# Kernel tuning notes

Hardware: AMD Instinct MI355X
Metric: run time of the kernel (lower is better)

Reference implementation:

```python
import jax, jax.numpy as jnp
import numpy as np

ROPE_BASE = 10000.0

def _rope_tables(T, head_dim, dtype):
    inv_freq = 1.0 / (ROPE_BASE ** (jnp.arange(0, head_dim, 2, dtype=jnp.float32) / head_dim))
    freqs = jnp.arange(T, dtype=jnp.float32)[:, None] * inv_freq[None, :]  # (T, hd/2)
    freqs = jnp.repeat(freqs, 2, axis=-1)  # (T, hd) interleaved (lucidrains-style)
    return jnp.cos(freqs).astype(dtype), jnp.sin(freqs).astype(dtype)

def _rotate_half(x):
    # interleaved pairs: (..., d) -> (-x2, x1) interleaved
    x = x.reshape(x.shape[:-1] + (-1, 2))
    x1, x2 = x[..., 0], x[..., 1]
    return jnp.stack((-x2, x1), axis=-1).reshape(x.shape[:-2] + (-1,))

def _apply_rope(x, cos, sin):
    # x: (B, H, T, hd); cos/sin: (T, hd)
    return x * cos[None, None] + _rotate_half(x) * sin[None, None]

def setup_inputs() -> dict:
    key = jax.random.key(0)
    k1, k2, k3 = jax.random.split(key, 3)
    B, T, C = 4, 2048, 1024
    x = jax.random.normal(k1, (B, T, C), dtype=jnp.float32)
    W_attn = jax.random.normal(k2, (C, 3 * C), dtype=jnp.float32) * 0.02
    W_proj = jax.random.normal(k3, (C, C), dtype=jnp.float32) * 0.02
    return {"x": x, "W_attn": W_attn, "W_proj": W_proj}

def reference(x, W_attn, W_proj):
    B, T, C = x.shape
    n_head = 16
    hd = C // n_head
    qkv = x @ W_attn  # (B, T, 3C)
    q, k, v = jnp.split(qkv, 3, axis=-1)
    # (B, T, H, hd) -> (B, H, T, hd)
    q = q.reshape(B, T, n_head, hd).transpose(0, 2, 1, 3)
    k = k.reshape(B, T, n_head, hd).transpose(0, 2, 1, 3)
    v = v.reshape(B, T, n_head, hd).transpose(0, 2, 1, 3)
    cos, sin = _rope_tables(T, hd, x.dtype)
    q = _apply_rope(q, cos, sin)
    k = _apply_rope(k, cos, sin)
    att = jnp.einsum('bhqd,bhkd->bhqk', q, k) * (1.0 / jnp.sqrt(jnp.array(hd, dtype=x.dtype)))
    causal = jnp.tril(jnp.ones((T, T), dtype=bool))
    att = jnp.where(causal[None, None], att, jnp.array(-jnp.inf, dtype=att.dtype))
    att = jax.nn.softmax(att, axis=-1)
    y = jnp.einsum('bhqk,bhkd->bhqd', att, v)
    y = y.transpose(0, 2, 1, 3).reshape(B, T, C)
    return y @ W_proj
```

## Files before the change

kernel.cpp:

```cpp
#include <hip/hip_runtime.h>
#include <hip/hip_bf16.h>
#include <math.h>

#define BB 4
#define TT 2048
#define CC 1024
#define NH 16
#define HD 64
#define C3 3072
#define LDK 72

#define QSCALE 0.18033688011112042f

typedef __attribute__((ext_vector_type(8))) short bf16x8;
typedef __attribute__((ext_vector_type(4))) float f32x4;

__device__ __forceinline__ void gload_lds16(const __hip_bfloat16* g, __hip_bfloat16* s) {
    __builtin_amdgcn_global_load_lds((const __attribute__((address_space(1))) void*)g,
                                     (__attribute__((address_space(3))) void*)s, 16, 0, 0);
}

__global__ __launch_bounds__(256) void rope_tables(float2* __restrict__ tab) {
    int idx = blockIdx.x * 256 + threadIdx.x;
    int t = idx >> 5;
    int p = idx & 31;
    float invf = exp2f((float)p * (-13.287712379549449f / 32.0f));
    float ang = (float)t * invf;
    float s, c;
    sincosf(ang, &s, &c);
    tab[idx] = make_float2(c, s);
}

__global__ __launch_bounds__(256) void cast_bf16x8(const float* __restrict__ X,
                                                   __hip_bfloat16* __restrict__ Y) {
    size_t i = ((size_t)blockIdx.x * 256 + threadIdx.x) * 8;
    float4 a = *(const float4*)(X + i);
    float4 b = *(const float4*)(X + i + 4);
    __align__(16) __hip_bfloat16 tmp[8];
    tmp[0] = __float2bfloat16(a.x);
    tmp[1] = __float2bfloat16(a.y);
    tmp[2] = __float2bfloat16(a.z);
    tmp[3] = __float2bfloat16(a.w);
    tmp[4] = __float2bfloat16(b.x);
    tmp[5] = __float2bfloat16(b.y);
    tmp[6] = __float2bfloat16(b.z);
    tmp[7] = __float2bfloat16(b.w);
    *(bf16x8*)(Y + i) = *(bf16x8*)tmp;
}

__global__ __launch_bounds__(256) void wtrans(const float* __restrict__ W,
                                              __hip_bfloat16* __restrict__ Wt,
                                              int K, int N) {
    __shared__ float st[64][65];
    const int n0 = blockIdx.x * 64;
    const int k0 = blockIdx.y * 64;
    const int tid = threadIdx.x;
    const int r = tid >> 4;
    const int c4 = (tid & 15) * 4;
#pragma unroll
    for (int p = 0; p < 4; ++p) {
        int k = p * 16 + r;
        float4 v = *(const float4*)(W + (size_t)(k0 + k) * N + n0 + c4);
        st[c4 + 0][k] = v.x;
        st[c4 + 1][k] = v.y;
        st[c4 + 2][k] = v.z;
        st[c4 + 3][k] = v.w;
    }
    __syncthreads();
    const int rr = tid >> 3;
    const int cc = (tid & 7) * 8;
#pragma unroll
    for (int p = 0; p < 2; ++p) {
        int n = p * 32 + rr;
        __align__(16) __hip_bfloat16 tmp[8];
#pragma unroll
        for (int j = 0; j < 8; ++j) tmp[j] = __float2bfloat16(st[n][cc + j]);
        *(bf16x8*)(Wt + (size_t)(n0 + n) * K + k0 + cc) = *(bf16x8*)tmp;
    }
}

#define CA0 0
#define CA1 1
#define CB0 2
#define CB1 3

#define BAR() __builtin_amdgcn_s_barrier()
#define SB0() __builtin_amdgcn_sched_barrier(0)
#define WAIT_LGKM0() do { asm volatile("s_waitcnt lgkmcnt(0)" ::: "memory"); SB0(); } while (0)
#define WAIT_VM4()   do { asm volatile("s_waitcnt vmcnt(4)" ::: "memory");  SB0(); } while (0)
#define WAIT_VM0()   do { asm volatile("s_waitcnt vmcnt(0)" ::: "memory");  SB0(); } while (0)

#define CLAMP_TS(x) ((x) < NTILE ? (x) : (x) - 2)

#define STAGE(gbase, h, ts, buf, cid) do {                                            \
    const __hip_bfloat16* _s = (gbase) + (size_t)((h) * 128 + w * 16) * K + (ts) * 64; \
    __hip_bfloat16* _d = &lds[buf][cid][w * 1024];                                    \
    gload_lds16(_s, _d);                                                              \
    gload_lds16(_s + 32, _d + 512);                                                   \
} while (0)

#define FRAGP(buf, cid, rowsub, ks)                                                   \
    ((const bf16x8*)((const char*)&lds[buf][cid][0] +                                 \
        (((rowsub) * 2 + (ks)) << 10) + (l16 << 6) + swzoff))

#define READ_A(buf, mi) do {                                                          \
    _Pragma("unroll") for (int _m = 0; _m < 4; ++_m)                                  \
    _Pragma("unroll") for (int _k = 0; _k < 2; ++_k)                                  \
        af[_m][_k] = *FRAGP(buf, wm, (mi) * 4 + _m, _k);                              \
} while (0)

#define READ_B(buf, ni) do {                                                          \
    _Pragma("unroll") for (int _n = 0; _n < 2; ++_n)                                  \
    _Pragma("unroll") for (int _k = 0; _k < 2; ++_k)                                  \
        bfr[(ni) * 2 + _n][_k] =                                                      \
            *FRAGP(buf, 2 + (wn >> 1), (wn & 1) * 4 + (ni) * 2 + _n, _k);             \
} while (0)

#define MFMA_Q(mb, nb) do {                                                           \
    __builtin_amdgcn_s_setprio(1);                                                    \
    _Pragma("unroll") for (int _m = 0; _m < 4; ++_m)                                  \
    _Pragma("unroll") for (int _n = 0; _n < 2; ++_n)                                  \
    _Pragma("unroll") for (int _k = 0; _k < 2; ++_k)                                  \
        acc[(mb) * 4 + _m][(nb) * 2 + _n] = __builtin_amdgcn_mfma_f32_16x16x32_bf16(  \
            af[_m][_k], bfr[(nb) * 2 + _n][_k], acc[(mb) * 4 + _m][(nb) * 2 + _n],    \
            0, 0, 0);                                                                 \
    __builtin_amdgcn_s_setprio(0);                                                    \
} while (0)

#define HALF_ITER(BUF, T12, B12, T34, B34) do {                                       \
                                                                 \
    READ_A(BUF, 0);                                                                   \
    READ_B(BUF, 0);                                                                   \
    STAGE(Bb, 1, CLAMP_TS(T12), B12, CB1);                                            \
    BAR(); WAIT_LGKM0();                                                              \
    MFMA_Q(0, 0);                                                                     \
    BAR();                                                                            \
                                                                 \
    READ_B(BUF, 1);                                                                   \
    STAGE(Ab, 1, CLAMP_TS(T12), B12, CA1);                                            \
    BAR(); WAIT_LGKM0();                                                              \
    MFMA_Q(0, 1);                                                                     \
    BAR();                                                                            \
                                                                 \
    READ_A(BUF, 1);                                                                   \
    STAGE(Bb, 0, CLAMP_TS(T34), B34, CB0);                                            \
    BAR(); WAIT_LGKM0();                                                              \
    MFMA_Q(1, 0);                                                                     \
    BAR();                                                                            \
                                                                 \
    STAGE(Ab, 0, CLAMP_TS(T34), B34, CA0);                                            \
    BAR(); WAIT_LGKM0();                                                              \
    MFMA_Q(1, 1);                                                                     \
    WAIT_VM4();                                                                       \
    BAR(); SB0();                                                                     \
} while (0)

#define GEMM256_BODY                                                                  \
    __shared__ __align__(16) __hip_bfloat16 lds[2][4][8192];             \
    const int tid = threadIdx.x;                                                      \
    const int w = tid >> 6;                                                           \
    const int lane = tid & 63;                                                        \
    const int l16 = lane & 15;                                                        \
    const int quad = lane >> 4;                                                       \
    const int wm = w >> 2;                                                            \
    const int wn = w & 3;                                                             \
    const int swzoff = ((quad * 8) ^ ((l16 & 8) << 1)) << 1;                          \
    const int bm0 = blockIdx.y * 256;                                                 \
    const int bn0 = blockIdx.x * 256;                                                 \
    const int NTILE = K >> 6;                                                         \
    const size_t laneOff = (size_t)(lane >> 2) * K +                                  \
                           (((lane & 3) * 8) ^ ((lane >> 5) << 4));                   \
    const __hip_bfloat16* Ab = A + (size_t)bm0 * K + laneOff;                         \
    const __hip_bfloat16* Bb = Bt + (size_t)bn0 * K + laneOff;                        \
    f32x4 acc[8][4] = {};                                                             \
             \
    STAGE(Bb, 0, 0, 0, CB0);                                                          \
    STAGE(Ab, 0, 0, 0, CA0);                                                          \
    STAGE(Bb, 1, 0, 0, CB1);                                                          \
    STAGE(Ab, 1, 0, 0, CA1);                                                          \
    STAGE(Bb, 0, 1, 1, CB0);                                                          \
    STAGE(Ab, 0, 1, 1, CA0);                                                          \
    WAIT_VM4();                                                                       \
    BAR(); SB0();                                                                     \
    for (int it = 0; it < NTILE / 2; ++it) {                                          \
        const int t = it * 2;                                                         \
        bf16x8 af[4][2], bfr[4][2];                                                   \
        HALF_ITER(0, t + 1, 1, t + 2, 0);                                             \
        HALF_ITER(1, t + 2, 0, t + 3, 1);                                             \
    }

__global__ __launch_bounds__(512) void gemm256_qkv_rope(const __hip_bfloat16* __restrict__ A,
                                                        const __hip_bfloat16* __restrict__ Bt,
                                                        const float2* __restrict__ tab,
                                                        __hip_bfloat16* __restrict__ C,
                                                        int M, int N, int K) {
    GEMM256_BODY

    if (bn0 < 2048) {
        const float qsc = (bn0 < 1024) ? QSCALE : 1.0f;
        const float sgn = (l16 & 1) ? 1.0f : -1.0f;
#pragma unroll
        for (int mt = 0; mt < 8; ++mt) {
            int row = bm0 + wm * 128 + mt * 16 + quad * 4;
#pragma unroll
            for (int nt = 0; nt < 4; ++nt) {
                int col = bn0 + wn * 64 + nt * 16 + l16;
                int p2 = nt * 8 + (l16 >> 1);
#pragma unroll
                for (int r = 0; r < 4; ++r) {
                    float own = acc[mt][nt][r];
                    float part = __shfl_xor(own, 1);
                    int trow = (row + r) & (TT - 1);
                    float2 cs = tab[(trow << 5) + p2];
                    float res = (own * cs.x + sgn * part * cs.y) * qsc;
                    C[(size_t)(row + r) * N + col] = __float2bfloat16(res);
                }
            }
        }
    } else {
#pragma unroll
        for (int mt = 0; mt < 8; ++mt) {
            int row = bm0 + wm * 128 + mt * 16 + quad * 4;
#pragma unroll
            for (int nt = 0; nt < 4; ++nt) {
                int col = bn0 + wn * 64 + nt * 16 + l16;
#pragma unroll
                for (int r = 0; r < 4; ++r)
                    C[(size_t)(row + r) * N + col] = __float2bfloat16(acc[mt][nt][r]);
            }
        }
    }
}

__global__ __launch_bounds__(512) void gemm256_f32(const __hip_bfloat16* __restrict__ A,
                                                   const __hip_bfloat16* __restrict__ Bt,
                                                   float* __restrict__ C,
                                                   int M, int N, int K) {
    GEMM256_BODY
#pragma unroll
    for (int mt = 0; mt < 8; ++mt) {
        int row = bm0 + wm * 128 + mt * 16 + quad * 4;
#pragma unroll
        for (int nt = 0; nt < 4; ++nt) {
            int col = bn0 + wn * 64 + nt * 16 + l16;
#pragma unroll
            for (int r = 0; r < 4; ++r)
                C[(size_t)(row + r) * N + col] = acc[mt][nt][r];
        }
    }
}

__global__ __launch_bounds__(256) void vtranspose(const __hip_bfloat16* __restrict__ qkvb,
                                                  __hip_bfloat16* __restrict__ vtb) {
    __shared__ __align__(16) __hip_bfloat16 st[64][LDK];
    const int bh = blockIdx.x >> 5;
    const int tt = blockIdx.x & 31;
    const int b = bh >> 4;
    const int h = bh & 15;
    const int tid = threadIdx.x;
    const int row = tid >> 3;
    const int col8 = (tid & 7) * 8;

#pragma unroll
    for (int pass = 0; pass < 2; ++pass) {
        int t = pass * 32 + row;
        *(bf16x8*)(&st[t][col8]) =
            *(const bf16x8*)(qkvb + ((size_t)(b * TT + tt * 64 + t)) * C3 + 2 * CC + h * HD + col8);
    }
    __syncthreads();
#pragma unroll
    for (int pass = 0; pass < 2; ++pass) {
        int d = pass * 32 + row;
        __align__(16) __hip_bfloat16 tmp[8];
#pragma unroll
        for (int j = 0; j < 8; ++j) tmp[j] = st[col8 + j][d];
        *(bf16x8*)(vtb + ((size_t)bh * HD + d) * TT + tt * 64 + col8) = *(bf16x8*)tmp;
    }
}

__global__ __launch_bounds__(256) void attn_mfma6(const __hip_bfloat16* __restrict__ qkvb,
                                                  const __hip_bfloat16* __restrict__ vtb,
                                                  __hip_bfloat16* __restrict__ y) {
    __shared__ __align__(16) __hip_bfloat16 Kb[3][64 * 64];
    __shared__ __align__(16) __hip_bfloat16 Vb[3][64 * 64];
    __shared__ __align__(16) __hip_bfloat16 Ps[4][2][16 * 72];

    const int tid = threadIdx.x;
    const int w = tid >> 6;
    const int lane = tid & 63;
    const int l16 = lane & 15;
    const int quad = lane >> 4;
    const int swz = l16 & 7;

    const int bh = blockIdx.x >> 3;
    const int pr = blockIdx.x & 7;
    const int b = bh >> 4;
    const int h = bh & 15;

    const int sr = (lane >> 3) & 7;
    const int sc = lane & 7;
    const int klog = (sc ^ sr) * 8;

    const __hip_bfloat16* kbase = qkvb + (size_t)b * TT * C3 + CC + h * HD + klog;
    const __hip_bfloat16* vbase = vtb + (size_t)bh * HD * TT + klog;

#define ATTN_STAGE(t, bidx) do {                                                  \
    _Pragma("unroll")                                                             \
    for (int half = 0; half < 2; ++half) {                                        \
        int kr = w * 16 + half * 8 + sr;                                          \
        gload_lds16(kbase + (size_t)((t) * 64 + kr) * C3,                         \
                    Kb[bidx] + (w * 16 + half * 8) * 64);                         \
        gload_lds16(vbase + (size_t)kr * TT + (t) * 64,                           \
                    Vb[bidx] + (w * 16 + half * 8) * 64);                         \
    }                                                                             \
} while (0)

#pragma unroll
    for (int seg = 0; seg < 2; ++seg) {
        const int qblk = (seg == 0) ? (15 - pr) : pr;
        const int qb = qblk * 128;
        const int jtmax = 2 * qblk + 1;
        const int qn0 = qb + w * 32;
        const int qn1 = qn0 + 16;

        bf16x8 qf[2][2];
#pragma unroll
        for (int qt = 0; qt < 2; ++qt) {
            const __hip_bfloat16* qp = qkvb + (size_t)(b * TT + qn0 + qt * 16 + l16) * C3 + h * HD;
            qf[qt][0] = *(const bf16x8*)(qp + quad * 8);
            qf[qt][1] = *(const bf16x8*)(qp + 32 + quad * 8);
        }

        f32x4 O[2][4] = {};
        float l_q[2] = {0.f, 0.f};

        __syncthreads();
        ATTN_STAGE(0, 0);
        ATTN_STAGE(1, 1);

        int bcur = 0;
        for (int jt = 0; jt <= jtmax; ++jt) {
            if (jt < jtmax) { WAIT_VM4(); } else { WAIT_VM0(); }
            BAR(); SB0();

            if (jt + 2 <= jtmax) {
                const int bs = (bcur >= 1) ? (bcur - 1) : 2;
                ATTN_STAGE(jt + 2, bs);
            }

            const __hip_bfloat16* Kp = Kb[bcur];
            const __hip_bfloat16* Vp = Vb[bcur];

            const bool sk0 = (jt * 64 > qn0 + 15);
            const bool sk1 = (jt * 64 > qn1 + 15);

            if (!sk1) {
                f32x4 St[2][4] = {};
                __builtin_amdgcn_s_setprio(1);
#pragma unroll
                for (int ks = 0; ks < 2; ++ks) {
#pragma unroll
                    for (int mt = 0; mt < 4; ++mt) {
                        bf16x8 kf = *(const bf16x8*)(Kp + (mt * 16 + l16) * 64 +
                                                     ((ks * 4 + quad) ^ swz) * 8);
                        St[0][mt] = __builtin_amdgcn_mfma_f32_16x16x32_bf16(kf, qf[0][ks], St[0][mt], 0, 0, 0);
                        St[1][mt] = __builtin_amdgcn_mfma_f32_16x16x32_bf16(kf, qf[1][ks], St[1][mt], 0, 0, 0);
                    }
                }
                __builtin_amdgcn_s_setprio(0);

#pragma unroll
                for (int qt = 0; qt < 2; ++qt) {
                    const bool skq = qt == 0 ? sk0 : sk1;
                    if (skq) continue;
                    const int qn = qt == 0 ? qn0 : qn1;
                    if (jt * 64 + 63 > qn) {
#pragma unroll
                        for (int mt = 0; mt < 4; ++mt) {
#pragma unroll
                            for (int r = 0; r < 4; ++r) {
                                int key = jt * 64 + mt * 16 + quad * 4 + r;
                                if (key > qn + l16) St[qt][mt][r] = -__builtin_inff();
                            }
                        }
                    }
                    float sum = 0.f;
#pragma unroll
                    for (int mt = 0; mt < 4; ++mt) {
                        float e0 = exp2f(St[qt][mt][0]);
                        float e1 = exp2f(St[qt][mt][1]);
                        float e2 = exp2f(St[qt][mt][2]);
                        float e3 = exp2f(St[qt][mt][3]);
                        sum += (e0 + e1) + (e2 + e3);
                        union { uint2 u; __hip_bfloat162 h[2]; } up;
                        up.h[0] = __float22bfloat162_rn(make_float2(e0, e1));
                        up.h[1] = __float22bfloat162_rn(make_float2(e2, e3));
                        *(uint2*)(&Ps[w][qt][l16 * 72 + mt * 16 + quad * 4]) = up.u;
                    }
                    l_q[qt] += sum;
                }

                bf16x8 vf[4][2];
#pragma unroll
                for (int dt = 0; dt < 4; ++dt) {
                    vf[dt][0] = *(const bf16x8*)(Vp + (dt * 16 + l16) * 64 + ((quad) ^ swz) * 8);
                    vf[dt][1] = *(const bf16x8*)(Vp + (dt * 16 + l16) * 64 + ((4 + quad) ^ swz) * 8);
                }
                __builtin_amdgcn_s_setprio(1);
#pragma unroll
                for (int qt = 0; qt < 2; ++qt) {
                    const bool skq = qt == 0 ? sk0 : sk1;
                    if (skq) continue;
                    bf16x8 pa0 = *(const bf16x8*)(&Ps[w][qt][l16 * 72 + quad * 8]);
                    bf16x8 pa1 = *(const bf16x8*)(&Ps[w][qt][l16 * 72 + 32 + quad * 8]);
#pragma unroll
                    for (int dt = 0; dt < 4; ++dt) {
                        O[qt][dt] = __builtin_amdgcn_mfma_f32_16x16x32_bf16(pa0, vf[dt][0], O[qt][dt], 0, 0, 0);
                        O[qt][dt] = __builtin_amdgcn_mfma_f32_16x16x32_bf16(pa1, vf[dt][1], O[qt][dt], 0, 0, 0);
                    }
                }
                __builtin_amdgcn_s_setprio(0);
            }

            bcur = (bcur == 2) ? 0 : bcur + 1;
        }

#pragma unroll
        for (int qt = 0; qt < 2; ++qt) {
            float l2 = l_q[qt];
            l2 += __shfl_xor(l2, 16);
            l2 += __shfl_xor(l2, 32);
            float lO[4];
#pragma unroll
            for (int r = 0; r < 4; ++r) lO[r] = 1.0f / __shfl(l2, quad * 4 + r);
            const int qbase = qn0 + qt * 16 + quad * 4;
#pragma unroll
            for (int dt = 0; dt < 4; ++dt) {
#pragma unroll
                for (int r = 0; r < 4; ++r) {
                    y[(size_t)(b * TT + qbase + r) * CC + h * HD + dt * 16 + l16] =
                        __float2bfloat16(O[qt][dt][r] * lO[r]);
                }
            }
        }
    }
#undef ATTN_STAGE
}

extern "C" void kernel_launch(void* const* d_in, const int* in_sizes, int n_in,
                              void* d_out, int out_size, void* d_ws, size_t ws_size,
                              hipStream_t stream) {
    const float* x      = (const float*)d_in[0];
    const float* W_attn = (const float*)d_in[1];
    const float* W_proj = (const float*)d_in[2];
    float* out = (float*)d_out;

    const size_t NBT = (size_t)BB * TT;
    __hip_bfloat16* xb   = (__hip_bfloat16*)d_ws;
    __hip_bfloat16* qkvb = xb + NBT * CC;
    __hip_bfloat16* vtb  = qkvb + NBT * C3;
    __hip_bfloat16* Wab  = vtb + NBT * CC;
    __hip_bfloat16* Wpb  = Wab + (size_t)CC * C3;
    float2* tab          = (float2*)(Wpb + (size_t)CC * CC);
    __hip_bfloat16* yb   = xb;

    const int M = BB * TT;

    rope_tables<<<dim3(TT * 32 / 256), 256, 0, stream>>>(tab);
    cast_bf16x8<<<dim3((int)(NBT * CC / 2048)), 256, 0, stream>>>(x, xb);
    wtrans<<<dim3(C3 / 64, CC / 64), 256, 0, stream>>>(W_attn, Wab, CC, C3);
    wtrans<<<dim3(CC / 64, CC / 64), 256, 0, stream>>>(W_proj, Wpb, CC, CC);

    gemm256_qkv_rope<<<dim3(C3 / 256, M / 256), 512, 0, stream>>>(xb, Wab, tab, qkvb, M, C3, CC);

    vtranspose<<<dim3(BB * NH * (TT / 64)), 256, 0, stream>>>(qkvb, vtb);

    attn_mfma6<<<dim3(BB * NH * 8), 256, 0, stream>>>(qkvb, vtb, yb);

    gemm256_f32<<<dim3(CC / 256, M / 256), 512, 0, stream>>>(yb, Wpb, out, M, CC, CC);
}
```

Before: 290.7 us.

## Split attention into 64-row query blocks with 2-wave workgroups and double buffering

Attention now launches 1024 workgroups of 128 threads, each handling two 64-row causal-paired query blocks instead of two 128-row blocks with 4 waves. K/V staging moves from triple to double buffering, with a second barrier before refilling, and the P tile buffer is shared per query tile. Block indices are remapped so adjacent workgroups go to different heads. The goal is more, smaller workgroups for better occupancy and load balance, at the cost of an extra barrier per tile and less prefetch depth.

```diff
diff --git a/kernel.cpp b/kernel.cpp
--- a/kernel.cpp
+++ b/kernel.cpp
@@ -88,6 +88,7 @@
 #define SB0() __builtin_amdgcn_sched_barrier(0)
 #define WAIT_LGKM0() do { asm volatile("s_waitcnt lgkmcnt(0)" ::: "memory"); SB0(); } while (0)
 #define WAIT_VM4()   do { asm volatile("s_waitcnt vmcnt(4)" ::: "memory");  SB0(); } while (0)
+#define WAIT_VM8()   do { asm volatile("s_waitcnt vmcnt(8)" ::: "memory");  SB0(); } while (0)
 #define WAIT_VM0()   do { asm volatile("s_waitcnt vmcnt(0)" ::: "memory");  SB0(); } while (0)
 
 #define CLAMP_TS(x) ((x) < NTILE ? (x) : (x) - 2)
@@ -278,12 +279,12 @@
     }
 }
 
-__global__ __launch_bounds__(256) void attn_mfma6(const __hip_bfloat16* __restrict__ qkvb,
+__global__ __launch_bounds__(128) void attn_mfma7(const __hip_bfloat16* __restrict__ qkvb,
                                                   const __hip_bfloat16* __restrict__ vtb,
                                                   __hip_bfloat16* __restrict__ y) {
-    __shared__ __align__(16) __hip_bfloat16 Kb[3][64 * 64];
-    __shared__ __align__(16) __hip_bfloat16 Vb[3][64 * 64];
-    __shared__ __align__(16) __hip_bfloat16 Ps[4][2][16 * 72];
+    __shared__ __align__(16) __hip_bfloat16 Kb[2][64 * 64];
+    __shared__ __align__(16) __hip_bfloat16 Vb[2][64 * 64];
+    __shared__ __align__(16) __hip_bfloat16 Ps[2][16 * 72];
 
     const int tid = threadIdx.x;
     const int w = tid >> 6;
@@ -292,8 +293,10 @@
     const int quad = lane >> 4;
     const int swz = l16 & 7;
 
-    const int bh = blockIdx.x >> 3;
-    const int pr = blockIdx.x & 7;
+    const int rb = blockIdx.x;
+    const int lb = (rb & 7) * 128 + (rb >> 3);
+    const int bh = lb >> 4;
+    const int g = lb & 15;
     const int b = bh >> 4;
     const int h = bh & 15;
 
@@ -306,21 +309,20 @@
 
 #define ATTN_STAGE(t, bidx) do {                                                  \
     _Pragma("unroll")                                                             \
-    for (int half = 0; half < 2; ++half) {                                        \
-        int kr = w * 16 + half * 8 + sr;                                          \
+    for (int hf = 0; hf < 4; ++hf) {                                              \
+        int kr = w * 32 + hf * 8 + sr;                                            \
         gload_lds16(kbase + (size_t)((t) * 64 + kr) * C3,                         \
-                    Kb[bidx] + (w * 16 + half * 8) * 64);                         \
+                    Kb[bidx] + (w * 32 + hf * 8) * 64);                           \
         gload_lds16(vbase + (size_t)kr * TT + (t) * 64,                           \
-                    Vb[bidx] + (w * 16 + half * 8) * 64);                         \
+                    Vb[bidx] + (w * 32 + hf * 8) * 64);                           \
     }                                                                             \
 } while (0)
 
 #pragma unroll
     for (int seg = 0; seg < 2; ++seg) {
-        const int qblk = (seg == 0) ? (15 - pr) : pr;
-        const int qb = qblk * 128;
-        const int jtmax = 2 * qblk + 1;
-        const int qn0 = qb + w * 32;
+        const int qrow0 = seg ? (TT - 64 * (g + 1)) : g * 64;
+        const int jtmax = seg ? (31 - g) : g;
+        const int qn0 = qrow0 + w * 32;
         const int qn1 = qn0 + 16;
 
         bf16x8 qf[2][2];
@@ -338,18 +340,13 @@
         ATTN_STAGE(0, 0);
         ATTN_STAGE(1, 1);
 
-        int bcur = 0;
         for (int jt = 0; jt <= jtmax; ++jt) {
-            if (jt < jtmax) { WAIT_VM4(); } else { WAIT_VM0(); }
+            if (jt < jtmax) { WAIT_VM8(); } else { WAIT_VM0(); }
             BAR(); SB0();
 
-            if (jt + 2 <= jtmax) {
-                const int bs = (bcur >= 1) ? (bcur - 1) : 2;
-                ATTN_STAGE(jt + 2, bs);
-            }
-
-            const __hip_bfloat16* Kp = Kb[bcur];
-            const __hip_bfloat16* Vp = Vb[bcur];
+            const int p = jt & 1;
+            const __hip_bfloat16* Kp = Kb[p];
+            const __hip_bfloat16* Vp = Vb[p];
 
             const bool sk0 = (jt * 64 > qn0 + 15);
             const bool sk1 = (jt * 64 > qn1 + 15);
@@ -368,6 +365,13 @@
                     }
                 }
                 __builtin_amdgcn_s_setprio(0);
+
+                bf16x8 vf[4][2];
+#pragma unroll
+                for (int dt = 0; dt < 4; ++dt) {
+                    vf[dt][0] = *(const bf16x8*)(Vp + (dt * 16 + l16) * 64 + ((quad) ^ swz) * 8);
+                    vf[dt][1] = *(const bf16x8*)(Vp + (dt * 16 + l16) * 64 + ((4 + quad) ^ swz) * 8);
+                }
 
 #pragma unroll
                 for (int qt = 0; qt < 2; ++qt) {
@@ -395,34 +399,26 @@
                         union { uint2 u; __hip_bfloat162 h[2]; } up;
                         up.h[0] = __float22bfloat162_rn(make_float2(e0, e1));
                         up.h[1] = __float22bfloat162_rn(make_float2(e2, e3));
-                        *(uint2*)(&Ps[w][qt][l16 * 72 + mt * 16 + quad * 4]) = up.u;
+                        *(uint2*)(&Ps[w][l16 * 72 + mt * 16 + quad * 4]) = up.u;
                     }
                     l_q[qt] += sum;
-                }
-
-                bf16x8 vf[4][2];
-#pragma unroll
-                for (int dt = 0; dt < 4; ++dt) {
-                    vf[dt][0] = *(const bf16x8*)(Vp + (dt * 16 + l16) * 64 + ((quad) ^ swz) * 8);
-                    vf[dt][1] = *(const bf16x8*)(Vp + (dt * 16 + l16) * 64 + ((4 + quad) ^ swz) * 8);
-                }
-                __builtin_amdgcn_s_setprio(1);
-#pragma unroll
-                for (int qt = 0; qt < 2; ++qt) {
-                    const bool skq = qt == 0 ? sk0 : sk1;
-                    if (skq) continue;
-                    bf16x8 pa0 = *(const bf16x8*)(&Ps[w][qt][l16 * 72 + quad * 8]);
-                    bf16x8 pa1 = *(const bf16x8*)(&Ps[w][qt][l16 * 72 + 32 + quad * 8]);
+
+                    bf16x8 pa0 = *(const bf16x8*)(&Ps[w][l16 * 72 + quad * 8]);
+                    bf16x8 pa1 = *(const bf16x8*)(&Ps[w][l16 * 72 + 32 + quad * 8]);
+                    __builtin_amdgcn_s_setprio(1);
 #pragma unroll
                     for (int dt = 0; dt < 4; ++dt) {
                         O[qt][dt] = __builtin_amdgcn_mfma_f32_16x16x32_bf16(pa0, vf[dt][0], O[qt][dt], 0, 0, 0);
                         O[qt][dt] = __builtin_amdgcn_mfma_f32_16x16x32_bf16(pa1, vf[dt][1], O[qt][dt], 0, 0, 0);
                     }
+                    __builtin_amdgcn_s_setprio(0);
                 }
-                __builtin_amdgcn_s_setprio(0);
             }
 
-            bcur = (bcur == 2) ? 0 : bcur + 1;
+            if (jt + 2 <= jtmax) {
+                BAR(); SB0();
+                ATTN_STAGE(jt + 2, p);
+            }
         }
 
 #pragma unroll
@@ -475,7 +471,7 @@
 
     vtranspose<<<dim3(BB * NH * (TT / 64)), 256, 0, stream>>>(qkvb, vtb);
 
-    attn_mfma6<<<dim3(BB * NH * 8), 256, 0, stream>>>(qkvb, vtb, yb);
+    attn_mfma7<<<dim3(BB * NH * 16), 128, 0, stream>>>(qkvb, vtb, yb);
 
     gemm256_f32<<<dim3(CC / 256, M / 256), 512, 0, stream>>>(yb, Wpb, out, M, CC, CC);
 }
```

New measurement: 315.3 us. 1.08x slower.

## Keep softmax P in registers by permuting V key order, remap attention blocks

Applied to the files above, without the earlier changes.

The transposed V is now written with a permuted key order within each 64-key tile. This lets the bf16 probability fragments produced by the QK^T MFMA output layout feed the PV MFMA directly from registers, so the per-warp LDS staging buffer for P is removed along with its store/load round trip. The PV MFMAs are also interleaved per query tile right after the exp computation. Separately, the block index is remapped so that the 8 query-pair blocks of the same head are spread across launch order, which changes load balance across CUs and L2 locality. Correctness depends on the key permutation matching the MFMA register layout exactly.

```diff
diff --git a/kernel.cpp b/kernel.cpp
--- a/kernel.cpp
+++ b/kernel.cpp
@@ -13,6 +13,7 @@
 #define QSCALE 0.18033688011112042f
 
 typedef __attribute__((ext_vector_type(8))) short bf16x8;
+typedef __attribute__((ext_vector_type(4))) short bf16x4;
 typedef __attribute__((ext_vector_type(4))) float f32x4;
 
 __device__ __forceinline__ void gload_lds16(const __hip_bfloat16* g, __hip_bfloat16* s) {
@@ -259,7 +260,8 @@
     const int h = bh & 15;
     const int tid = threadIdx.x;
     const int row = tid >> 3;
-    const int col8 = (tid & 7) * 8;
+    const int a = tid & 7;
+    const int col8 = a * 8;
 
 #pragma unroll
     for (int pass = 0; pass < 2; ++pass) {
@@ -268,22 +270,27 @@
             *(const bf16x8*)(qkvb + ((size_t)(b * TT + tt * 64 + t)) * C3 + 2 * CC + h * HD + col8);
     }
     __syncthreads();
+    const int h32 = (a >> 2) & 1;
+    const int m4  = (a >> 1) & 1;
+    const int p0 = h32 * 32 + ((2 * a) & 3) * 8 + m4 * 4;
+    const int p1 = h32 * 32 + ((2 * a + 1) & 3) * 8 + m4 * 4;
 #pragma unroll
     for (int pass = 0; pass < 2; ++pass) {
         int d = pass * 32 + row;
         __align__(16) __hip_bfloat16 tmp[8];
 #pragma unroll
         for (int j = 0; j < 8; ++j) tmp[j] = st[col8 + j][d];
-        *(bf16x8*)(vtb + ((size_t)bh * HD + d) * TT + tt * 64 + col8) = *(bf16x8*)tmp;
-    }
-}
-
-__global__ __launch_bounds__(256) void attn_mfma6(const __hip_bfloat16* __restrict__ qkvb,
+        __hip_bfloat16* dst = vtb + ((size_t)bh * HD + d) * TT + tt * 64;
+        *(bf16x4*)(dst + p0) = *(const bf16x4*)&tmp[0];
+        *(bf16x4*)(dst + p1) = *(const bf16x4*)&tmp[4];
+    }
+}
+
+__global__ __launch_bounds__(256) void attn_mfma9(const __hip_bfloat16* __restrict__ qkvb,
                                                   const __hip_bfloat16* __restrict__ vtb,
                                                   __hip_bfloat16* __restrict__ y) {
     __shared__ __align__(16) __hip_bfloat16 Kb[3][64 * 64];
     __shared__ __align__(16) __hip_bfloat16 Vb[3][64 * 64];
-    __shared__ __align__(16) __hip_bfloat16 Ps[4][2][16 * 72];
 
     const int tid = threadIdx.x;
     const int w = tid >> 6;
@@ -292,8 +299,10 @@
     const int quad = lane >> 4;
     const int swz = l16 & 7;
 
-    const int bh = blockIdx.x >> 3;
-    const int pr = blockIdx.x & 7;
+    const int rb = blockIdx.x;
+    const int lb = (rb & 7) * 64 + (rb >> 3);
+    const int bh = lb >> 3;
+    const int pr = lb & 7;
     const int b = bh >> 4;
     const int h = bh & 15;
 
@@ -369,6 +378,13 @@
                 }
                 __builtin_amdgcn_s_setprio(0);
 
+                bf16x8 vf[4][2];
+#pragma unroll
+                for (int dt = 0; dt < 4; ++dt) {
+                    vf[dt][0] = *(const bf16x8*)(Vp + (dt * 16 + l16) * 64 + ((quad) ^ swz) * 8);
+                    vf[dt][1] = *(const bf16x8*)(Vp + (dt * 16 + l16) * 64 + ((4 + quad) ^ swz) * 8);
+                }
+
 #pragma unroll
                 for (int qt = 0; qt < 2; ++qt) {
                     const bool skq = qt == 0 ? sk0 : sk1;
@@ -385,6 +401,7 @@
                         }
                     }
                     float sum = 0.f;
+                    union { bf16x8 v; __hip_bfloat162 hh[4]; } pk0, pk1;
 #pragma unroll
                     for (int mt = 0; mt < 4; ++mt) {
                         float e0 = exp2f(St[qt][mt][0]);
@@ -392,34 +409,21 @@
                         float e2 = exp2f(St[qt][mt][2]);
                         float e3 = exp2f(St[qt][mt][3]);
                         sum += (e0 + e1) + (e2 + e3);
-                        union { uint2 u; __hip_bfloat162 h[2]; } up;
-                        up.h[0] = __float22bfloat162_rn(make_float2(e0, e1));
-                        up.h[1] = __float22bfloat162_rn(make_float2(e2, e3));
-                        *(uint2*)(&Ps[w][qt][l16 * 72 + mt * 16 + quad * 4]) = up.u;
+                        __hip_bfloat162 lo = __float22bfloat162_rn(make_float2(e0, e1));
+                        __hip_bfloat162 hi = __float22bfloat162_rn(make_float2(e2, e3));
+                        if (mt < 2) { pk0.hh[mt * 2] = lo; pk0.hh[mt * 2 + 1] = hi; }
+                        else        { pk1.hh[(mt - 2) * 2] = lo; pk1.hh[(mt - 2) * 2 + 1] = hi; }
                     }
                     l_q[qt] += sum;
+
+                    __builtin_amdgcn_s_setprio(1);
+#pragma unroll
+                    for (int dt = 0; dt < 4; ++dt) {
+                        O[qt][dt] = __builtin_amdgcn_mfma_f32_16x16x32_bf16(pk0.v, vf[dt][0], O[qt][dt], 0, 0, 0);
+                        O[qt][dt] = __builtin_amdgcn_mfma_f32_16x16x32_bf16(pk1.v, vf[dt][1], O[qt][dt], 0, 0, 0);
+                    }
+                    __builtin_amdgcn_s_setprio(0);
                 }
-
-                bf16x8 vf[4][2];
-#pragma unroll
-                for (int dt = 0; dt < 4; ++dt) {
-                    vf[dt][0] = *(const bf16x8*)(Vp + (dt * 16 + l16) * 64 + ((quad) ^ swz) * 8);
-                    vf[dt][1] = *(const bf16x8*)(Vp + (dt * 16 + l16) * 64 + ((4 + quad) ^ swz) * 8);
-                }
-                __builtin_amdgcn_s_setprio(1);
-#pragma unroll
-                for (int qt = 0; qt < 2; ++qt) {
-                    const bool skq = qt == 0 ? sk0 : sk1;
-                    if (skq) continue;
-                    bf16x8 pa0 = *(const bf16x8*)(&Ps[w][qt][l16 * 72 + quad * 8]);
-                    bf16x8 pa1 = *(const bf16x8*)(&Ps[w][qt][l16 * 72 + 32 + quad * 8]);
-#pragma unroll
-                    for (int dt = 0; dt < 4; ++dt) {
-                        O[qt][dt] = __builtin_amdgcn_mfma_f32_16x16x32_bf16(pa0, vf[dt][0], O[qt][dt], 0, 0, 0);
-                        O[qt][dt] = __builtin_amdgcn_mfma_f32_16x16x32_bf16(pa1, vf[dt][1], O[qt][dt], 0, 0, 0);
-                    }
-                }
-                __builtin_amdgcn_s_setprio(0);
             }
 
             bcur = (bcur == 2) ? 0 : bcur + 1;
@@ -475,7 +479,7 @@
 
     vtranspose<<<dim3(BB * NH * (TT / 64)), 256, 0, stream>>>(qkvb, vtb);
 
-    attn_mfma6<<<dim3(BB * NH * 8), 256, 0, stream>>>(qkvb, vtb, yb);
+    attn_mfma9<<<dim3(BB * NH * 8), 256, 0, stream>>>(qkvb, vtb, yb);
 
     gemm256_f32<<<dim3(CC / 256, M / 256), 512, 0, stream>>>(yb, Wpb, out, M, CC, CC);
 }
```

Measured after the change: 281.8 us. 3.1% less time.
